# Kernel optimization log

Measured on AMD Instinct MI355X. Metric: run time of the kernel, lower is better.

The kernel has to match this reference:

```python
import jax, jax.numpy as jnp
import numpy as np

DIM = 256
NUM_HEADS = 8
CHUNK = 64
EPS = 1e-5


def layernorm(x, g, b):
    m = jnp.mean(x, axis=-1, keepdims=True)
    v = jnp.mean((x - m) ** 2, axis=-1, keepdims=True)
    return (x - m) / jnp.sqrt(v + EPS) * g + b


def setup_inputs() -> dict:
    key = jax.random.key(0)
    ks = jax.random.split(key, 12)
    B, C, H, W = 8, DIM, 64, 64
    s = 1.0 / np.sqrt(C)
    return {
        "x": jax.random.normal(ks[0], (B, C, H, W), jnp.float32),
        "CVA_input": jax.random.normal(ks[1], (B, C, H, W), jnp.float32),
        "qn_g": jnp.ones((C,), jnp.float32), "qn_b": jnp.zeros((C,), jnp.float32),
        "kn_g": jnp.ones((C,), jnp.float32), "kn_b": jnp.zeros((C,), jnp.float32),
        "vn_g": jnp.ones((C,), jnp.float32), "vn_b": jnp.zeros((C,), jnp.float32),
        "Wq": jax.random.normal(ks[2], (C, C), jnp.float32) * s,
        "bq": jnp.zeros((C,), jnp.float32),
        "Wk": jax.random.normal(ks[3], (C, C), jnp.float32) * s,
        "bk": jnp.zeros((C,), jnp.float32),
        "Wv": jax.random.normal(ks[4], (C, C), jnp.float32) * s,
        "bv": jnp.zeros((C,), jnp.float32),
        "Wp": jax.random.normal(ks[5], (C, C), jnp.float32) * s,
        "bp": jnp.zeros((C,), jnp.float32),
    }


def reference(x, CVA_input, qn_g, qn_b, kn_g, kn_b, vn_g, vn_b,
              Wq, bq, Wk, bk, Wv, bv, Wp, bp):
    B, C, H, W = x.shape
    N = H * W
    nh = NUM_HEADS
    hd = C // nh
    scale = hd ** -0.5
    nc = N // CHUNK  # number of non-overlapping chunks

    xs = x.reshape(B, C, N).transpose(0, 2, 1)          # [B,N,C]
    cva = CVA_input.reshape(B, -1, C)                    # [B,N,C] (raw reshape, as in torch)

    def heads(t):  # [B,N,C] -> [B,nh,nc,CHUNK,hd]
        return t.reshape(B, N, nh, hd).transpose(0, 2, 1, 3).reshape(B, nh, nc, CHUNK, hd)

    q = heads(layernorm(cva, qn_g, qn_b) @ Wq + bq)
    k = heads(layernorm(cva, kn_g, kn_b) @ Wk + bk)
    v = heads(layernorm(xs, vn_g, vn_b) @ Wv + bv)

    # block-local attention: each chunk attends only within itself
    scores = jnp.einsum('bhncd,bhnkd->bhnck', q, k) * scale  # [B,nh,nc,CHUNK,CHUNK]
    probs = jax.nn.softmax(scores, axis=-1)
    o = jnp.einsum('bhnck,bhnkd->bhncd', probs, v)           # [B,nh,nc,CHUNK,hd]

    o = o.reshape(B, nh, N, hd).transpose(0, 2, 1, 3).reshape(B, N, C)
    out = o @ Wp + bp                                        # [B,N,C]
    return out.transpose(0, 2, 1).reshape(B, C, H, W)
```

## Files before the change

### kernel.cpp

```cpp
#include <hip/hip_runtime.h>
#include <hip/hip_bf16.h>

#define NTOK 4096
#define BATCH 8
#define NROWS (BATCH * NTOK)

typedef __attribute__((ext_vector_type(8))) short bfx8;
typedef __attribute__((ext_vector_type(4))) short bfx4;
typedef __attribute__((ext_vector_type(4))) float f32x4;

__device__ __forceinline__ short f2bf(float f) {
    unsigned u = __builtin_bit_cast(unsigned, f);
    u += 0x7fffu + ((u >> 16) & 1u);
    return (short)(u >> 16);
}

#define MFMA16(a, b, c) __builtin_amdgcn_mfma_f32_16x16x32_bf16(a, b, c, 0, 0, 0)

__global__ __launch_bounds__(256) void prep_w(
    const float* __restrict__ Wq, const float* __restrict__ Wk,
    const float* __restrict__ Wv, const float* __restrict__ Wp,
    const float* __restrict__ qg, const float* __restrict__ qb,
    const float* __restrict__ kg, const float* __restrict__ kb,
    const float* __restrict__ vg, const float* __restrict__ vb,
    short* __restrict__ wt, float* __restrict__ bbp) {
    int m = blockIdx.x;
    int ci0 = blockIdx.y * 16;
    const float *W, *g, *be;
    float scale = 1.0f;
    if (m == 0)      { W = Wq; g = qg; be = qb; scale = 0.17677669529663687f; }
    else if (m == 1) { W = Wk; g = kg; be = kb; }
    else if (m == 2) { W = Wv; g = vg; be = vb; }
    else             { W = Wp; g = nullptr; be = nullptr; }
    __shared__ float tile[16][257];
    int t = threadIdx.x;
#pragma unroll
    for (int i = 0; i < 16; i++)
        tile[i][t] = W[(size_t)(ci0 + i) * 256 + t];
    __syncthreads();
    float p = 0.f;
    if (be) {
#pragma unroll
        for (int i = 0; i < 16; i++) p += be[ci0 + i] * tile[i][t];
    }
    bbp[(m * 16 + blockIdx.y) * 256 + t] = p;
    short* WT = wt + m * 65536 + t * 256 + ci0;
    bfx8 o0, o1;
#pragma unroll
    for (int j = 0; j < 8; j++) {
        float gv = g ? g[ci0 + j] : 1.0f;
        o0[j] = f2bf(scale * gv * tile[j][t]);
    }
#pragma unroll
    for (int j = 0; j < 8; j++) {
        float gv = g ? g[ci0 + 8 + j] : 1.0f;
        o1[j] = f2bf(scale * gv * tile[8 + j][t]);
    }
    *reinterpret_cast<bfx8*>(WT) = o0;
    *reinterpret_cast<bfx8*>(WT + 8) = o1;
}

__global__ __launch_bounds__(256) void prep_b(
    const float* __restrict__ bq, const float* __restrict__ bk,
    const float* __restrict__ bv, const float* __restrict__ bp,
    const float* __restrict__ bbp, float* __restrict__ bb) {
    int m = blockIdx.x, t = threadIdx.x;
    const float* bias = (m == 0) ? bq : (m == 1) ? bk : (m == 2) ? bv : bp;
    float scale = (m == 0) ? 0.17677669529663687f : 1.0f;
    float s = bias[t];
#pragma unroll
    for (int i = 0; i < 16; i++) s += bbp[(m * 16 + i) * 256 + t];
    bb[m * 256 + t] = scale * s;
}

__global__ __launch_bounds__(512) void mega(const float* __restrict__ x,
                                            const float* __restrict__ cva,
                                            const short* __restrict__ wt,
                                            const float* __restrict__ bb,
                                            float* __restrict__ out) {
    int id = blockIdx.x;
    int b = id >> 6, ch = id & 63;
    int t = threadIdx.x, w = t >> 6, l = t & 63, c = l & 15, g = l >> 4;
    int h = w;

    __shared__ short lds[4 * 64 * 264];
    __shared__ float red[8][64][2];
    short* A    = lds;
    short* B    = lds + 16896;
    short* Cs   = lds + 2 * 16896;
    short* D    = lds + 3 * 16896;
    short* Preg = B;

    const float* xb   = x + (size_t)b * 1048576 + ch * 64;
    const float* cvab = cva + (size_t)(b * 4096 + ch * 64) * 256;

    float xg[32];
#pragma unroll
    for (int i = 0; i < 32; i++) xg[i] = xb[(size_t)(w * 32 + i) * 4096 + l];

#pragma unroll
    for (int i = 0; i < 8; i++) {
        int row = w * 8 + i;
        float4 v = *reinterpret_cast<const float4*>(cvab + (size_t)row * 256 + l * 4);
        float s = v.x + v.y + v.z + v.w;
        float q2 = v.x * v.x + v.y * v.y + v.z * v.z + v.w * v.w;
#pragma unroll
        for (int m = 1; m < 64; m <<= 1) { s += __shfl_xor(s, m); q2 += __shfl_xor(q2, m); }
        float mean = s * (1.0f / 256.0f);
        float var  = q2 * (1.0f / 256.0f) - mean * mean;
        float rstd = rsqrtf(var + 1e-5f);
        bfx4 o;
        o[0] = f2bf((v.x - mean) * rstd);
        o[1] = f2bf((v.y - mean) * rstd);
        o[2] = f2bf((v.z - mean) * rstd);
        o[3] = f2bf((v.w - mean) * rstd);
        *reinterpret_cast<bfx4*>(A + row * 264 + l * 4) = o;
    }

    {
        float s = 0.f, q2 = 0.f;
#pragma unroll
        for (int i = 0; i < 32; i++) { s += xg[i]; q2 += xg[i] * xg[i]; }
        red[w][l][0] = s;
        red[w][l][1] = q2;
    }
    __syncthreads();

    float xmean, xrstd;
    {
        float s = 0.f, q2 = 0.f;
#pragma unroll
        for (int j2 = 0; j2 < 8; j2++) { s += red[j2][l][0]; q2 += red[j2][l][1]; }
        xmean = s * (1.0f / 256.0f);
        xrstd = rsqrtf(q2 * (1.0f / 256.0f) - xmean * xmean + 1e-5f);
    }

    {
        f32x4 qacc[4][2] = {}, kacc[4][2] = {};
        const short* wq0 = wt + (size_t)(w * 32 + c) * 256 + g * 8;
        const short* wq1 = wq0 + 16 * 256;
        const short* wk0 = wq0 + 65536;
        const short* wk1 = wq1 + 65536;
#pragma unroll
        for (int ks = 0; ks < 8; ks++) {
            bfx8 af[4];
#pragma unroll
            for (int m = 0; m < 4; m++)
                af[m] = *reinterpret_cast<const bfx8*>(A + (m * 16 + c) * 264 + ks * 32 + g * 8);
            bfx8 q0 = *reinterpret_cast<const bfx8*>(wq0 + ks * 32);
            bfx8 q1 = *reinterpret_cast<const bfx8*>(wq1 + ks * 32);
            bfx8 k0 = *reinterpret_cast<const bfx8*>(wk0 + ks * 32);
            bfx8 k1 = *reinterpret_cast<const bfx8*>(wk1 + ks * 32);
#pragma unroll
            for (int m = 0; m < 4; m++) {
                qacc[m][0] = MFMA16(af[m], q0, qacc[m][0]);
                qacc[m][1] = MFMA16(af[m], q1, qacc[m][1]);
                kacc[m][0] = MFMA16(af[m], k0, kacc[m][0]);
                kacc[m][1] = MFMA16(af[m], k1, kacc[m][1]);
            }
        }
        float bq0 = bb[w * 32 + c], bq1 = bb[w * 32 + 16 + c];
        float bk0 = bb[256 + w * 32 + c], bk1 = bb[256 + w * 32 + 16 + c];
#pragma unroll
        for (int m = 0; m < 4; m++)
#pragma unroll
            for (int j = 0; j < 4; j++) {
                int row = m * 16 + g * 4 + j;
                B [row * 264 + w * 32 + c]      = f2bf(qacc[m][0][j] + bq0);
                B [row * 264 + w * 32 + 16 + c] = f2bf(qacc[m][1][j] + bq1);
                Cs[row * 264 + w * 32 + c]      = f2bf(kacc[m][0][j] + bk0);
                Cs[row * 264 + w * 32 + 16 + c] = f2bf(kacc[m][1][j] + bk1);
            }
    }
    __syncthreads();

#pragma unroll
    for (int i2 = 0; i2 < 4; i2++) {
        bfx8 o;
#pragma unroll
        for (int jj = 0; jj < 8; jj++) o[jj] = f2bf((xg[i2 * 8 + jj] - xmean) * xrstd);
        *reinterpret_cast<bfx8*>(A + l * 264 + w * 32 + i2 * 8) = o;
    }
    __syncthreads();

    {
        f32x4 vacc[4][2] = {};
        const short* wv0 = wt + 2 * 65536 + (size_t)(w * 32 + c) * 256 + g * 8;
        const short* wv1 = wv0 + 16 * 256;
#pragma unroll
        for (int ks = 0; ks < 8; ks++) {
            bfx8 af[4];
#pragma unroll
            for (int m = 0; m < 4; m++)
                af[m] = *reinterpret_cast<const bfx8*>(A + (m * 16 + c) * 264 + ks * 32 + g * 8);
            bfx8 v0 = *reinterpret_cast<const bfx8*>(wv0 + ks * 32);
            bfx8 v1 = *reinterpret_cast<const bfx8*>(wv1 + ks * 32);
#pragma unroll
            for (int m = 0; m < 4; m++) {
                vacc[m][0] = MFMA16(af[m], v0, vacc[m][0]);
                vacc[m][1] = MFMA16(af[m], v1, vacc[m][1]);
            }
        }
        float bv0 = bb[512 + w * 32 + c], bv1 = bb[512 + w * 32 + 16 + c];
#pragma unroll
        for (int m = 0; m < 4; m++)
#pragma unroll
            for (int j = 0; j < 4; j++) {
                int row = m * 16 + g * 4 + j;
                D[row * 264 + w * 32 + c]      = f2bf(vacc[m][0][j] + bv0);
                D[row * 264 + w * 32 + 16 + c] = f2bf(vacc[m][1][j] + bv1);
            }
    }

    f32x4 s[4][4] = {};
    {
        bfx8 qf[4], kf[4];
#pragma unroll
        for (int m = 0; m < 4; m++)
            qf[m] = *reinterpret_cast<const bfx8*>(B + (m * 16 + c) * 264 + h * 32 + g * 8);
#pragma unroll
        for (int n = 0; n < 4; n++)
            kf[n] = *reinterpret_cast<const bfx8*>(Cs + (n * 16 + c) * 264 + h * 32 + g * 8);
#pragma unroll
        for (int m = 0; m < 4; m++)
#pragma unroll
            for (int n = 0; n < 4; n++)
                s[m][n] = MFMA16(qf[m], kf[n], s[m][n]);
    }
    float rs[4][4];
#pragma unroll
    for (int m = 0; m < 4; m++)
#pragma unroll
        for (int j = 0; j < 4; j++) {
            float mx = fmaxf(fmaxf(s[m][0][j], s[m][1][j]), fmaxf(s[m][2][j], s[m][3][j]));
            mx = fmaxf(mx, __shfl_xor(mx, 1));
            mx = fmaxf(mx, __shfl_xor(mx, 2));
            mx = fmaxf(mx, __shfl_xor(mx, 4));
            mx = fmaxf(mx, __shfl_xor(mx, 8));
            float sum = 0.f;
#pragma unroll
            for (int n = 0; n < 4; n++) {
                float e = __expf(s[m][n][j] - mx);
                s[m][n][j] = e;
                sum += e;
            }
            sum += __shfl_xor(sum, 1);
            sum += __shfl_xor(sum, 2);
            sum += __shfl_xor(sum, 4);
            sum += __shfl_xor(sum, 8);
            rs[m][j] = 1.0f / sum;
        }
    __syncthreads();

    {
        short* Phs = Preg + h * 4096;
        const char* Phc = (const char*)Phs;
#pragma unroll
        for (int m = 0; m < 4; m++)
#pragma unroll
            for (int n = 0; n < 4; n++)
#pragma unroll
                for (int j = 0; j < 4; j++) {
                    int row = m * 16 + g * 4 + j;
                    int sw = (row & 7) << 4;
                    Phs[row * 64 + ((((n * 16 + c) << 1) ^ sw) >> 1)] = f2bf(s[m][n][j]);
                }
        __builtin_amdgcn_s_waitcnt(0);

        f32x4 oacc[4][2] = {};
#pragma unroll
        for (int ks = 0; ks < 2; ks++) {
            bfx8 vf[2];
#pragma unroll
            for (int n2 = 0; n2 < 2; n2++)
#pragma unroll
                for (int jj = 0; jj < 8; jj++)
                    vf[n2][jj] = D[(ks * 32 + g * 8 + jj) * 264 + h * 32 + n2 * 16 + c];
#pragma unroll
            for (int m = 0; m < 4; m++) {
                int row = m * 16 + c;
                int sw = (row & 7) << 4;
                bfx8 pf = *reinterpret_cast<const bfx8*>(Phc + row * 128 + ((ks * 64 + g * 16) ^ sw));
#pragma unroll
                for (int n2 = 0; n2 < 2; n2++)
                    oacc[m][n2] = MFMA16(pf, vf[n2], oacc[m][n2]);
            }
        }
#pragma unroll
        for (int m = 0; m < 4; m++)
#pragma unroll
            for (int n2 = 0; n2 < 2; n2++)
#pragma unroll
                for (int j = 0; j < 4; j++)
                    A[(m * 16 + g * 4 + j) * 264 + h * 32 + n2 * 16 + c] =
                        f2bf(oacc[m][n2][j] * rs[m][j]);
    }
    __syncthreads();

    {
        f32x4 pacc[4][2] = {};
        const short* wp0 = wt + 3 * 65536 + (size_t)(w * 32 + c) * 256 + g * 8;
        const short* wp1 = wp0 + 16 * 256;
#pragma unroll
        for (int ks = 0; ks < 8; ks++) {
            bfx8 af[4];
#pragma unroll
            for (int m = 0; m < 4; m++)
                af[m] = *reinterpret_cast<const bfx8*>(A + (m * 16 + c) * 264 + ks * 32 + g * 8);
            bfx8 p0 = *reinterpret_cast<const bfx8*>(wp0 + ks * 32);
            bfx8 p1 = *reinterpret_cast<const bfx8*>(wp1 + ks * 32);
#pragma unroll
            for (int m = 0; m < 4; m++) {
                pacc[m][0] = MFMA16(af[m], p0, pacc[m][0]);
                pacc[m][1] = MFMA16(af[m], p1, pacc[m][1]);
            }
        }
        float* trw = reinterpret_cast<float*>(Preg + h * 4096);
        float* outb = out + (size_t)b * 1048576 + ch * 64;
#pragma unroll
        for (int p = 0; p < 2; p++) {
            float bv = bb[768 + w * 32 + p * 16 + c];
#pragma unroll
            for (int m = 0; m < 4; m++)
#pragma unroll
                for (int j = 0; j < 4; j++)
                    trw[c * 65 + m * 16 + g * 4 + j] = pacc[m][p][j] + bv;
            __builtin_amdgcn_s_waitcnt(0);
#pragma unroll
            for (int cl = 0; cl < 16; cl++) {
                int co = w * 32 + p * 16 + cl;
                outb[(size_t)co * 4096 + l] = trw[cl * 65 + l];
            }
            __builtin_amdgcn_s_waitcnt(0);
        }
    }
}

extern "C" void kernel_launch(void* const* d_in, const int* in_sizes, int n_in,
                              void* d_out, int out_size, void* d_ws, size_t ws_size,
                              hipStream_t stream) {
    const float* x   = (const float*)d_in[0];
    const float* cva = (const float*)d_in[1];
    const float* qg  = (const float*)d_in[2];
    const float* qb  = (const float*)d_in[3];
    const float* kg  = (const float*)d_in[4];
    const float* kb  = (const float*)d_in[5];
    const float* vg  = (const float*)d_in[6];
    const float* vb  = (const float*)d_in[7];
    const float* Wq  = (const float*)d_in[8];
    const float* bq  = (const float*)d_in[9];
    const float* Wk  = (const float*)d_in[10];
    const float* bk  = (const float*)d_in[11];
    const float* Wv  = (const float*)d_in[12];
    const float* bv  = (const float*)d_in[13];
    const float* Wp  = (const float*)d_in[14];
    const float* bp  = (const float*)d_in[15];
    float* out = (float*)d_out;
    char* ws = (char*)d_ws;

    short* wt  = (short*)(ws);
    float* bb  = (float*)(ws + 4 * 65536 * sizeof(short));
    float* bbp = bb + 1024;

    prep_w<<<dim3(4, 16), 256, 0, stream>>>(Wq, Wk, Wv, Wp, qg, qb, kg, kb, vg, vb,
                                            wt, bbp);
    prep_b<<<4, 256, 0, stream>>>(bq, bk, bv, bp, bbp, bb);

    mega<<<512, 512, 0, stream>>>(x, cva, wt, bb, out);
}
```

Baseline: 79.37 us.

## Shrink LDS footprint with per-wave scratch and transposed attention

```diff
diff --git a/kernel.cpp b/kernel.cpp
--- a/kernel.cpp
+++ b/kernel.cpp
@@ -14,8 +14,16 @@
     u += 0x7fffu + ((u >> 16) & 1u);
     return (short)(u >> 16);
 }
+__device__ __forceinline__ unsigned pk2(float a, float b) {
+    return (unsigned)(unsigned short)f2bf(a) | ((unsigned)(unsigned short)f2bf(b) << 16);
+}
 
 #define MFMA16(a, b, c) __builtin_amdgcn_mfma_f32_16x16x32_bf16(a, b, c, 0, 0, 0)
+#define LGKM0()                                              \
+    do {                                                     \
+        asm volatile("s_waitcnt lgkmcnt(0)" ::: "memory");   \
+        __builtin_amdgcn_sched_barrier(0);                   \
+    } while (0)
 
 __global__ __launch_bounds__(256) void prep_w(
     const float* __restrict__ Wq, const float* __restrict__ Wk,
@@ -73,30 +81,22 @@
     bb[m * 256 + t] = scale * s;
 }
 
-__global__ __launch_bounds__(512) void mega(const float* __restrict__ x,
-                                            const float* __restrict__ cva,
-                                            const short* __restrict__ wt,
-                                            const float* __restrict__ bb,
-                                            float* __restrict__ out) {
+__global__ __launch_bounds__(512, 4) void mega(const float* __restrict__ x,
+                                               const float* __restrict__ cva,
+                                               const short* __restrict__ wt,
+                                               const float* __restrict__ bb,
+                                               float* __restrict__ out) {
     int id = blockIdx.x;
     int b = id >> 6, ch = id & 63;
     int t = threadIdx.x, w = t >> 6, l = t & 63, c = l & 15, g = l >> 4;
-    int h = w;
-
-    __shared__ short lds[4 * 64 * 264];
+
+    __shared__ short A[64 * 264];
+    __shared__ short scr_[8][2560];
     __shared__ float red[8][64][2];
-    short* A    = lds;
-    short* B    = lds + 16896;
-    short* Cs   = lds + 2 * 16896;
-    short* D    = lds + 3 * 16896;
-    short* Preg = B;
+    short* S = scr_[w];
 
     const float* xb   = x + (size_t)b * 1048576 + ch * 64;
     const float* cvab = cva + (size_t)(b * 4096 + ch * 64) * 256;
-
-    float xg[32];
-#pragma unroll
-    for (int i = 0; i < 32; i++) xg[i] = xb[(size_t)(w * 32 + i) * 4096 + l];
 
 #pragma unroll
     for (int i = 0; i < 8; i++) {
@@ -107,8 +107,7 @@
 #pragma unroll
         for (int m = 1; m < 64; m <<= 1) { s += __shfl_xor(s, m); q2 += __shfl_xor(q2, m); }
         float mean = s * (1.0f / 256.0f);
-        float var  = q2 * (1.0f / 256.0f) - mean * mean;
-        float rstd = rsqrtf(var + 1e-5f);
+        float rstd = rsqrtf(q2 * (1.0f / 256.0f) - mean * mean + 1e-5f);
         bfx4 o;
         o[0] = f2bf((v.x - mean) * rstd);
         o[1] = f2bf((v.y - mean) * rstd);
@@ -116,6 +115,84 @@
         o[3] = f2bf((v.w - mean) * rstd);
         *reinterpret_cast<bfx4*>(A + row * 264 + l * 4) = o;
     }
+    __syncthreads();
+
+    f32x4 qa[4][2] = {};
+    {
+        const short* w0 = wt + (size_t)(w * 32 + c) * 256 + g * 8;
+        const short* w1 = w0 + 16 * 256;
+#pragma unroll
+        for (int ks = 0; ks < 8; ks++) {
+            bfx8 af[4];
+#pragma unroll
+            for (int m = 0; m < 4; m++)
+                af[m] = *reinterpret_cast<const bfx8*>(A + (m * 16 + c) * 264 + ks * 32 + g * 8);
+            bfx8 q0 = *reinterpret_cast<const bfx8*>(w0 + ks * 32);
+            bfx8 q1 = *reinterpret_cast<const bfx8*>(w1 + ks * 32);
+#pragma unroll
+            for (int m = 0; m < 4; m++) {
+                qa[m][0] = MFMA16(af[m], q0, qa[m][0]);
+                qa[m][1] = MFMA16(af[m], q1, qa[m][1]);
+            }
+        }
+    }
+    bfx8 qf[4];
+    {
+        float b0 = bb[w * 32 + c], b1 = bb[w * 32 + 16 + c];
+#pragma unroll
+        for (int m = 0; m < 4; m++)
+#pragma unroll
+            for (int j = 0; j < 4; j++) {
+                S[(m * 16 + g * 4 + j) * 40 + c]      = f2bf(qa[m][0][j] + b0);
+                S[(m * 16 + g * 4 + j) * 40 + 16 + c] = f2bf(qa[m][1][j] + b1);
+            }
+        LGKM0();
+#pragma unroll
+        for (int np = 0; np < 4; np++)
+            qf[np] = *reinterpret_cast<const bfx8*>(S + (np * 16 + c) * 40 + g * 8);
+        LGKM0();
+    }
+
+    f32x4 ka[4][2] = {};
+    {
+        const short* w0 = wt + 65536 + (size_t)(w * 32 + c) * 256 + g * 8;
+        const short* w1 = w0 + 16 * 256;
+#pragma unroll
+        for (int ks = 0; ks < 8; ks++) {
+            bfx8 af[4];
+#pragma unroll
+            for (int m = 0; m < 4; m++)
+                af[m] = *reinterpret_cast<const bfx8*>(A + (m * 16 + c) * 264 + ks * 32 + g * 8);
+            bfx8 k0 = *reinterpret_cast<const bfx8*>(w0 + ks * 32);
+            bfx8 k1 = *reinterpret_cast<const bfx8*>(w1 + ks * 32);
+#pragma unroll
+            for (int m = 0; m < 4; m++) {
+                ka[m][0] = MFMA16(af[m], k0, ka[m][0]);
+                ka[m][1] = MFMA16(af[m], k1, ka[m][1]);
+            }
+        }
+    }
+
+    float xg[32];
+#pragma unroll
+    for (int i = 0; i < 32; i++) xg[i] = xb[(size_t)(w * 32 + i) * 4096 + l];
+
+    bfx8 kf[4];
+    {
+        float b0 = bb[256 + w * 32 + c], b1 = bb[256 + w * 32 + 16 + c];
+#pragma unroll
+        for (int m = 0; m < 4; m++)
+#pragma unroll
+            for (int j = 0; j < 4; j++) {
+                S[(m * 16 + g * 4 + j) * 40 + c]      = f2bf(ka[m][0][j] + b0);
+                S[(m * 16 + g * 4 + j) * 40 + 16 + c] = f2bf(ka[m][1][j] + b1);
+            }
+        LGKM0();
+#pragma unroll
+        for (int m = 0; m < 4; m++)
+            kf[m] = *reinterpret_cast<const bfx8*>(S + (m * 16 + c) * 40 + g * 8);
+        LGKM0();
+    }
 
     {
         float s = 0.f, q2 = 0.f;
@@ -135,203 +212,164 @@
         xrstd = rsqrtf(q2 * (1.0f / 256.0f) - xmean * xmean + 1e-5f);
     }
 
-    {
-        f32x4 qacc[4][2] = {}, kacc[4][2] = {};
-        const short* wq0 = wt + (size_t)(w * 32 + c) * 256 + g * 8;
-        const short* wq1 = wq0 + 16 * 256;
-        const short* wk0 = wq0 + 65536;
-        const short* wk1 = wq1 + 65536;
+#pragma unroll
+    for (int i2 = 0; i2 < 4; i2++) {
+        bfx8 o;
+#pragma unroll
+        for (int jj = 0; jj < 8; jj++) o[jj] = f2bf((xg[i2 * 8 + jj] - xmean) * xrstd);
+        *reinterpret_cast<bfx8*>(A + l * 264 + w * 32 + i2 * 8) = o;
+    }
+    __syncthreads();
+
+    f32x4 sa[4][4] = {};
+#pragma unroll
+    for (int m = 0; m < 4; m++)
+#pragma unroll
+        for (int np = 0; np < 4; np++)
+            sa[m][np] = MFMA16(kf[m], qf[np], sa[m][np]);
+
+    float rs[4];
+#pragma unroll
+    for (int np = 0; np < 4; np++) {
+        float mx = sa[0][np][0];
+#pragma unroll
+        for (int m = 0; m < 4; m++)
+#pragma unroll
+            for (int j = 0; j < 4; j++) mx = fmaxf(mx, sa[m][np][j]);
+        mx = fmaxf(mx, __shfl_xor(mx, 16));
+        mx = fmaxf(mx, __shfl_xor(mx, 32));
+        float sum = 0.f;
+#pragma unroll
+        for (int m = 0; m < 4; m++)
+#pragma unroll
+            for (int j = 0; j < 4; j++) {
+                float e = __expf(sa[m][np][j] - mx);
+                sa[m][np][j] = e;
+                sum += e;
+            }
+        sum += __shfl_xor(sum, 16);
+        sum += __shfl_xor(sum, 32);
+        rs[np] = 1.0f / sum;
+    }
+
+    unsigned Pp[4][4][2];
+#pragma unroll
+    for (int m = 0; m < 4; m++)
+#pragma unroll
+        for (int np = 0; np < 4; np++) {
+            Pp[m][np][0] = pk2(sa[m][np][0], sa[m][np][1]);
+            Pp[m][np][1] = pk2(sa[m][np][2], sa[m][np][3]);
+        }
+
+    f32x4 va[4][2] = {};
+    {
+        const short* w0 = wt + 2 * 65536 + (size_t)(w * 32 + c) * 256 + g * 8;
+        const short* w1 = w0 + 16 * 256;
 #pragma unroll
         for (int ks = 0; ks < 8; ks++) {
             bfx8 af[4];
 #pragma unroll
             for (int m = 0; m < 4; m++)
                 af[m] = *reinterpret_cast<const bfx8*>(A + (m * 16 + c) * 264 + ks * 32 + g * 8);
-            bfx8 q0 = *reinterpret_cast<const bfx8*>(wq0 + ks * 32);
-            bfx8 q1 = *reinterpret_cast<const bfx8*>(wq1 + ks * 32);
-            bfx8 k0 = *reinterpret_cast<const bfx8*>(wk0 + ks * 32);
-            bfx8 k1 = *reinterpret_cast<const bfx8*>(wk1 + ks * 32);
+            bfx8 v0 = *reinterpret_cast<const bfx8*>(w0 + ks * 32);
+            bfx8 v1 = *reinterpret_cast<const bfx8*>(w1 + ks * 32);
 #pragma unroll
             for (int m = 0; m < 4; m++) {
-                qacc[m][0] = MFMA16(af[m], q0, qacc[m][0]);
-                qacc[m][1] = MFMA16(af[m], q1, qacc[m][1]);
-                kacc[m][0] = MFMA16(af[m], k0, kacc[m][0]);
-                kacc[m][1] = MFMA16(af[m], k1, kacc[m][1]);
-            }
-        }
-        float bq0 = bb[w * 32 + c], bq1 = bb[w * 32 + 16 + c];
-        float bk0 = bb[256 + w * 32 + c], bk1 = bb[256 + w * 32 + 16 + c];
+                va[m][0] = MFMA16(af[m], v0, va[m][0]);
+                va[m][1] = MFMA16(af[m], v1, va[m][1]);
+            }
+        }
+    }
+    __syncthreads();
+
+    bfx8 vf[2][2];
+    {
+        float b0 = bb[512 + w * 32 + c], b1 = bb[512 + w * 32 + 16 + c];
 #pragma unroll
         for (int m = 0; m < 4; m++)
 #pragma unroll
             for (int j = 0; j < 4; j++) {
-                int row = m * 16 + g * 4 + j;
-                B [row * 264 + w * 32 + c]      = f2bf(qacc[m][0][j] + bq0);
-                B [row * 264 + w * 32 + 16 + c] = f2bf(qacc[m][1][j] + bq1);
-                Cs[row * 264 + w * 32 + c]      = f2bf(kacc[m][0][j] + bk0);
-                Cs[row * 264 + w * 32 + 16 + c] = f2bf(kacc[m][1][j] + bk1);
-            }
-    }
-    __syncthreads();
-
-#pragma unroll
-    for (int i2 = 0; i2 < 4; i2++) {
-        bfx8 o;
-#pragma unroll
-        for (int jj = 0; jj < 8; jj++) o[jj] = f2bf((xg[i2 * 8 + jj] - xmean) * xrstd);
-        *reinterpret_cast<bfx8*>(A + l * 264 + w * 32 + i2 * 8) = o;
-    }
-    __syncthreads();
-
-    {
-        f32x4 vacc[4][2] = {};
-        const short* wv0 = wt + 2 * 65536 + (size_t)(w * 32 + c) * 256 + g * 8;
-        const short* wv1 = wv0 + 16 * 256;
+                S[c * 72 + m * 16 + g * 4 + j]        = f2bf(va[m][0][j] + b0);
+                S[(16 + c) * 72 + m * 16 + g * 4 + j] = f2bf(va[m][1][j] + b1);
+            }
+        LGKM0();
+#pragma unroll
+        for (int ks = 0; ks < 2; ks++)
+#pragma unroll
+            for (int mD = 0; mD < 2; mD++)
+                vf[ks][mD] = *reinterpret_cast<const bfx8*>(S + (mD * 16 + c) * 72 + ks * 32 + g * 8);
+        LGKM0();
+    }
+
+    f32x4 oa[2][4] = {};
+#pragma unroll
+    for (int ks = 0; ks < 2; ks++) {
+#pragma unroll
+        for (int m2 = 0; m2 < 2; m2++)
+#pragma unroll
+            for (int np = 0; np < 4; np++) {
+                *reinterpret_cast<unsigned*>(S + (np * 16 + c) * 40 + m2 * 16 + g * 4)     = Pp[ks * 2 + m2][np][0];
+                *reinterpret_cast<unsigned*>(S + (np * 16 + c) * 40 + m2 * 16 + g * 4 + 2) = Pp[ks * 2 + m2][np][1];
+            }
+        LGKM0();
+        bfx8 pf[4];
+#pragma unroll
+        for (int np = 0; np < 4; np++)
+            pf[np] = *reinterpret_cast<const bfx8*>(S + (np * 16 + c) * 40 + g * 8);
+        LGKM0();
+#pragma unroll
+        for (int mD = 0; mD < 2; mD++)
+#pragma unroll
+            for (int np = 0; np < 4; np++)
+                oa[mD][np] = MFMA16(vf[ks][mD], pf[np], oa[mD][np]);
+    }
+
+#pragma unroll
+    for (int mD = 0; mD < 2; mD++)
+#pragma unroll
+        for (int np = 0; np < 4; np++) {
+            bfx4 o4;
+#pragma unroll
+            for (int j = 0; j < 4; j++) o4[j] = f2bf(oa[mD][np][j] * rs[np]);
+            *reinterpret_cast<bfx4*>(A + (np * 16 + c) * 264 + w * 32 + mD * 16 + g * 4) = o4;
+        }
+    __syncthreads();
+
+    {
+        f32x4 pa[4][2] = {};
+        const short* w0 = wt + 3 * 65536 + (size_t)(w * 32 + c) * 256 + g * 8;
+        const short* w1 = w0 + 16 * 256;
 #pragma unroll
         for (int ks = 0; ks < 8; ks++) {
             bfx8 af[4];
 #pragma unroll
             for (int m = 0; m < 4; m++)
                 af[m] = *reinterpret_cast<const bfx8*>(A + (m * 16 + c) * 264 + ks * 32 + g * 8);
-            bfx8 v0 = *reinterpret_cast<const bfx8*>(wv0 + ks * 32);
-            bfx8 v1 = *reinterpret_cast<const bfx8*>(wv1 + ks * 32);
+            bfx8 p0 = *reinterpret_cast<const bfx8*>(w0 + ks * 32);
+            bfx8 p1 = *reinterpret_cast<const bfx8*>(w1 + ks * 32);
 #pragma unroll
             for (int m = 0; m < 4; m++) {
-                vacc[m][0] = MFMA16(af[m], v0, vacc[m][0]);
-                vacc[m][1] = MFMA16(af[m], v1, vacc[m][1]);
-            }
-        }
-        float bv0 = bb[512 + w * 32 + c], bv1 = bb[512 + w * 32 + 16 + c];
-#pragma unroll
-        for (int m = 0; m < 4; m++)
-#pragma unroll
-            for (int j = 0; j < 4; j++) {
-                int row = m * 16 + g * 4 + j;
-                D[row * 264 + w * 32 + c]      = f2bf(vacc[m][0][j] + bv0);
-                D[row * 264 + w * 32 + 16 + c] = f2bf(vacc[m][1][j] + bv1);
-            }
-    }
-
-    f32x4 s[4][4] = {};
-    {
-        bfx8 qf[4], kf[4];
-#pragma unroll
-        for (int m = 0; m < 4; m++)
-            qf[m] = *reinterpret_cast<const bfx8*>(B + (m * 16 + c) * 264 + h * 32 + g * 8);
-#pragma unroll
-        for (int n = 0; n < 4; n++)
-            kf[n] = *reinterpret_cast<const bfx8*>(Cs + (n * 16 + c) * 264 + h * 32 + g * 8);
-#pragma unroll
-        for (int m = 0; m < 4; m++)
-#pragma unroll
-            for (int n = 0; n < 4; n++)
-                s[m][n] = MFMA16(qf[m], kf[n], s[m][n]);
-    }
-    float rs[4][4];
-#pragma unroll
-    for (int m = 0; m < 4; m++)
-#pragma unroll
-        for (int j = 0; j < 4; j++) {
-            float mx = fmaxf(fmaxf(s[m][0][j], s[m][1][j]), fmaxf(s[m][2][j], s[m][3][j]));
-            mx = fmaxf(mx, __shfl_xor(mx, 1));
-            mx = fmaxf(mx, __shfl_xor(mx, 2));
-            mx = fmaxf(mx, __shfl_xor(mx, 4));
-            mx = fmaxf(mx, __shfl_xor(mx, 8));
-            float sum = 0.f;
-#pragma unroll
-            for (int n = 0; n < 4; n++) {
-                float e = __expf(s[m][n][j] - mx);
-                s[m][n][j] = e;
-                sum += e;
-            }
-            sum += __shfl_xor(sum, 1);
-            sum += __shfl_xor(sum, 2);
-            sum += __shfl_xor(sum, 4);
-            sum += __shfl_xor(sum, 8);
-            rs[m][j] = 1.0f / sum;
-        }
-    __syncthreads();
-
-    {
-        short* Phs = Preg + h * 4096;
-        const char* Phc = (const char*)Phs;
-#pragma unroll
-        for (int m = 0; m < 4; m++)
-#pragma unroll
-            for (int n = 0; n < 4; n++)
-#pragma unroll
-                for (int j = 0; j < 4; j++) {
-                    int row = m * 16 + g * 4 + j;
-                    int sw = (row & 7) << 4;
-                    Phs[row * 64 + ((((n * 16 + c) << 1) ^ sw) >> 1)] = f2bf(s[m][n][j]);
-                }
-        __builtin_amdgcn_s_waitcnt(0);
-
-        f32x4 oacc[4][2] = {};
-#pragma unroll
-        for (int ks = 0; ks < 2; ks++) {
-            bfx8 vf[2];
-#pragma unroll
-            for (int n2 = 0; n2 < 2; n2++)
-#pragma unroll
-                for (int jj = 0; jj < 8; jj++)
-                    vf[n2][jj] = D[(ks * 32 + g * 8 + jj) * 264 + h * 32 + n2 * 16 + c];
-#pragma unroll
-            for (int m = 0; m < 4; m++) {
-                int row = m * 16 + c;
-                int sw = (row & 7) << 4;
-                bfx8 pf = *reinterpret_cast<const bfx8*>(Phc + row * 128 + ((ks * 64 + g * 16) ^ sw));
-#pragma unroll
-                for (int n2 = 0; n2 < 2; n2++)
-                    oacc[m][n2] = MFMA16(pf, vf[n2], oacc[m][n2]);
-            }
-        }
-#pragma unroll
-        for (int m = 0; m < 4; m++)
-#pragma unroll
-            for (int n2 = 0; n2 < 2; n2++)
+                pa[m][0] = MFMA16(af[m], p0, pa[m][0]);
+                pa[m][1] = MFMA16(af[m], p1, pa[m][1]);
+            }
+        }
+        float* trw = reinterpret_cast<float*>(S);
+        float* outb = out + (size_t)b * 1048576 + ch * 64;
+#pragma unroll
+        for (int p = 0; p < 2; p++) {
+            float bvv = bb[768 + w * 32 + p * 16 + c];
+#pragma unroll
+            for (int m = 0; m < 4; m++)
 #pragma unroll
                 for (int j = 0; j < 4; j++)
-                    A[(m * 16 + g * 4 + j) * 264 + h * 32 + n2 * 16 + c] =
-                        f2bf(oacc[m][n2][j] * rs[m][j]);
-    }
-    __syncthreads();
-
-    {
-        f32x4 pacc[4][2] = {};
-        const short* wp0 = wt + 3 * 65536 + (size_t)(w * 32 + c) * 256 + g * 8;
-        const short* wp1 = wp0 + 16 * 256;
-#pragma unroll
-        for (int ks = 0; ks < 8; ks++) {
-            bfx8 af[4];
-#pragma unroll
-            for (int m = 0; m < 4; m++)
-                af[m] = *reinterpret_cast<const bfx8*>(A + (m * 16 + c) * 264 + ks * 32 + g * 8);
-            bfx8 p0 = *reinterpret_cast<const bfx8*>(wp0 + ks * 32);
-            bfx8 p1 = *reinterpret_cast<const bfx8*>(wp1 + ks * 32);
-#pragma unroll
-            for (int m = 0; m < 4; m++) {
-                pacc[m][0] = MFMA16(af[m], p0, pacc[m][0]);
-                pacc[m][1] = MFMA16(af[m], p1, pacc[m][1]);
-            }
-        }
-        float* trw = reinterpret_cast<float*>(Preg + h * 4096);
-        float* outb = out + (size_t)b * 1048576 + ch * 64;
-#pragma unroll
-        for (int p = 0; p < 2; p++) {
-            float bv = bb[768 + w * 32 + p * 16 + c];
-#pragma unroll
-            for (int m = 0; m < 4; m++)
-#pragma unroll
-                for (int j = 0; j < 4; j++)
-                    trw[c * 65 + m * 16 + g * 4 + j] = pacc[m][p][j] + bv;
-            __builtin_amdgcn_s_waitcnt(0);
+                    trw[c * 65 + m * 16 + g * 4 + j] = pa[m][p][j] + bvv;
+            LGKM0();
 #pragma unroll
             for (int cl = 0; cl < 16; cl++) {
                 int co = w * 32 + p * 16 + cl;
                 outb[(size_t)co * 4096 + l] = trw[cl * 65 + l];
             }
-            __builtin_amdgcn_s_waitcnt(0);
+            LGKM0();
         }
     }
 }
```

Result: faster. 67.76 us (-14.6%).
